# Kernel optimization log

Hardware: AMD Instinct MI355X
Metric: run time of the kernel (lower is better)

## Reference

```python
import jax, jax.numpy as jnp
import numpy as np

B, L, D, H = 2, 4096, 128, 4


def setup_inputs() -> dict:
    key = jax.random.key(0)
    k_x, k_q, k_k, k_v, k_o = jax.random.split(key, 5)
    std = 0.02
    x = jax.random.normal(k_x, (B, L, D), dtype=jnp.float32)
    # torch nn.Linear(d_model, H*d_model).weight has shape [H*D, D]
    Wq = std * jax.random.normal(k_q, (H * D, D), dtype=jnp.float32)
    Wk = std * jax.random.normal(k_k, (H * D, D), dtype=jnp.float32)
    Wv = std * jax.random.normal(k_v, (H * D, D), dtype=jnp.float32)
    # W_O: Linear(H*d_model, d_model).weight -> [D, H*D]
    Wo = std * jax.random.normal(k_o, (D, H * D), dtype=jnp.float32)
    return {"x": x, "Wq": Wq, "Wk": Wk, "Wv": Wv, "Wo": Wo}


def reference(x, Wq, Wk, Wv, Wo):
    # project: weight rows indexed by (h, e); out = x @ W^T
    Wq3 = Wq.reshape(H, D, D)
    Wk3 = Wk.reshape(H, D, D)
    Wv3 = Wv.reshape(H, D, D)
    q = jnp.einsum('bld,hed->bhle', x, Wq3)  # [B,H,L,D]
    k = jnp.einsum('bld,hed->bhle', x, Wk3)
    v = jnp.einsum('bld,hed->bhle', x, Wv3)
    logits = jnp.einsum('bhle,bhme->bhlm', q, k)  # [B,H,L,L]
    causal_mask = jnp.triu(jnp.ones((L, L), dtype=bool), 1)
    neg = jnp.finfo(logits.dtype).min
    logits = jnp.where(causal_mask, neg, logits)
    attn = jax.nn.softmax(logits, axis=-1)
    ctx = jnp.einsum('bhlm,bhme->bhle', attn, v)  # [B,H,L,D]
    ctx = ctx.transpose(0, 2, 1, 3).reshape(B, L, H * D)
    y = ctx @ Wo.T  # [B,L,D]
    return y
```

## Files before the change

### kernel.cpp

```cpp
#include <hip/hip_runtime.h>
#include <hip/hip_bf16.h>

#define BB 2
#define LL 4096
#define DD 128
#define HH 4

typedef unsigned short u16;
typedef unsigned int u32;
typedef __attribute__((ext_vector_type(8))) short short8;
typedef __attribute__((ext_vector_type(4))) float floatx4;

union PFrag { short8 s; u32 u[4]; };

__device__ __forceinline__ u16 f2bf(float f) {
    union { float f; u32 u; } v; v.f = f;
    return (u16)((v.u + 0x7fffu + ((v.u >> 16) & 1u)) >> 16);
}

__device__ __forceinline__ float bf2f(u16 u) {
    union { u32 u; float f; } v; v.u = (u32)u << 16;
    return v.f;
}

__device__ __forceinline__ u32 pk2bf(float a, float b) {
    union { __hip_bfloat162 h; u32 u; } v;
    v.h = __float22bfloat162_rn(float2{a, b});
    return v.u;
}

__device__ __forceinline__ void gld16(const u16* g, u16* l) {
    __builtin_amdgcn_global_load_lds((const __attribute__((address_space(1))) void*)g,
                                     (__attribute__((address_space(3))) void*)l, 16, 0, 0);
}

__device__ __forceinline__ int pfx2(int t) {
    int a = t >> 2, b = t & 3;
    return 2 * a * (a - 1) + a * b;
}

__global__ __launch_bounds__(256) void cvt_all(const float* __restrict__ x,
                                               const float* __restrict__ wq,
                                               const float* __restrict__ wk,
                                               const float* __restrict__ wv,
                                               const float* __restrict__ wo,
                                               u16* xb, u16* wqb, u16* wkb,
                                               u16* wvb, u16* wob,
                                               float* l_acc) {
    int z = blockIdx.y;
    if (z == 5) {
        int i = (blockIdx.x * 256 + threadIdx.x) * 4;
        if (i < 8 * LL) *(float4*)(l_acc + i) = (float4){0.f, 0.f, 0.f, 0.f};
        return;
    }
    const float* src; u16* dst; int n;
    if      (z == 0) { src = x;  dst = xb;  n = BB * LL * DD; }
    else if (z == 1) { src = wq; dst = wqb; n = HH * DD * DD; }
    else if (z == 2) { src = wk; dst = wkb; n = HH * DD * DD; }
    else if (z == 3) { src = wv; dst = wvb; n = HH * DD * DD; }
    else             { src = wo; dst = wob; n = DD * HH * DD; }
    int i = (blockIdx.x * 256 + threadIdx.x) * 4;
    if (i >= n) return;
    float4 v = *(const float4*)(src + i);
    ushort4 o;
    o.x = f2bf(v.x); o.y = f2bf(v.y); o.z = f2bf(v.z); o.w = f2bf(v.w);
    *(ushort4*)(dst + i) = o;
}

__global__ __launch_bounds__(256) void proj_qkv(const u16* __restrict__ xb,
                                                const u16* __restrict__ wqb,
                                                const u16* __restrict__ wkb,
                                                const u16* __restrict__ wvb,
                                                u16* __restrict__ Qb,
                                                u16* __restrict__ Kb,
                                                u16* __restrict__ Vt) {
    __shared__ __align__(16) u16 At[128 * 128];
    __shared__ __align__(16) u16 Wt[128 * 128];
    int lane = threadIdx.x & 63;
    int w    = threadIdx.x >> 6;
    int c = lane & 15, g = lane >> 4;
    int mt = blockIdx.x;
    int nt = blockIdx.y;
    int z = nt >> 2, h = nt & 3;
    const u16* Wg = ((z == 0) ? wqb : (z == 1) ? wkb : wvb) + h * 128 * DD;
    const u16* Ag = xb + (size_t)mt * 128 * DD;

#pragma unroll
    for (int i = 0; i < 8; i++) {
        int row = i * 16 + w * 4 + (lane >> 4);
        int cc  = (lane & 15) ^ (row & 15);
        gld16(Ag + row * DD + cc * 8, &At[(i * 16 + w * 4) * 128]);
    }
#pragma unroll
    for (int i = 0; i < 8; i++) {
        int row = i * 16 + w * 4 + (lane >> 4);
        int cc  = (lane & 15) ^ (row & 15);
        gld16(Wg + row * DD + cc * 8, &Wt[(i * 16 + w * 4) * 128]);
    }
    __syncthreads();

    const u16* Abuf = (z < 2) ? At : Wt;
    const u16* Bbuf = (z < 2) ? Wt : At;

    floatx4 acc[2][8];
#pragma unroll
    for (int m2 = 0; m2 < 2; m2++)
#pragma unroll
        for (int n2 = 0; n2 < 8; n2++) acc[m2][n2] = (floatx4){0.f, 0.f, 0.f, 0.f};

#pragma unroll
    for (int kk = 0; kk < 4; kk++) {
        short8 a0, a1, bf[8];
        {
            int r0 = w * 32 + c;
            int r1 = r0 + 16;
            a0 = *(const short8*)(&Abuf[r0 * 128 + (((g + 4 * kk) ^ (r0 & 15)) * 8)]);
            a1 = *(const short8*)(&Abuf[r1 * 128 + (((g + 4 * kk) ^ (r1 & 15)) * 8)]);
        }
#pragma unroll
        for (int n2 = 0; n2 < 8; n2++) {
            int rn = n2 * 16 + c;
            bf[n2] = *(const short8*)(&Bbuf[rn * 128 + (((g + 4 * kk) ^ (rn & 15)) * 8)]);
        }
#pragma unroll
        for (int n2 = 0; n2 < 8; n2++) {
            acc[0][n2] = __builtin_amdgcn_mfma_f32_16x16x32_bf16(a0, bf[n2], acc[0][n2], 0, 0, 0);
            acc[1][n2] = __builtin_amdgcn_mfma_f32_16x16x32_bf16(a1, bf[n2], acc[1][n2], 0, 0, 0);
        }
    }

    if (z < 2) {
        u16* out = (z == 0) ? Qb : Kb;
#pragma unroll
        for (int m2 = 0; m2 < 2; m2++)
#pragma unroll
            for (int r = 0; r < 4; r++) {
                int lg = mt * 128 + w * 32 + m2 * 16 + g * 4 + r;
                int b_ = lg >> 12, l = lg & 4095;
                u16* op = out + ((size_t)(b_ * HH + h) * LL + l) * DD + c;
#pragma unroll
                for (int n2 = 0; n2 < 8; n2++) op[n2 * 16] = f2bf(acc[m2][n2][r]);
            }
    } else {
        int b_ = mt >> 5;
        int lbase = (mt & 31) * 128;
#pragma unroll
        for (int m2 = 0; m2 < 2; m2++)
#pragma unroll
            for (int r = 0; r < 4; r++) {
                int e = w * 32 + m2 * 16 + g * 4 + r;
                u16* op = Vt + ((size_t)(b_ * HH + h) * DD + e) * LL + lbase + c;
#pragma unroll
                for (int n2 = 0; n2 < 8; n2++) op[n2 * 16] = f2bf(acc[m2][n2][r]);
            }
    }
}

__global__ __launch_bounds__(256, 3) void flash_attn(const u16* __restrict__ Q,
                                                     const u16* __restrict__ K,
                                                     const u16* __restrict__ Vt,
                                                     u16* __restrict__ basep,
                                                     u16* __restrict__ slots,
                                                     float* __restrict__ l_acc) {
    __shared__ __align__(16) u16 Kls[2][32 * 128];
    __shared__ __align__(16) u16 Vls[2][512 * 8];

    int lane = threadIdx.x & 63;
    int w    = threadIdx.x >> 6;
    int c = lane & 15, g = lane >> 4;

    int bid  = blockIdx.x;
    int head = bid & 7;
    int i    = bid >> 3;
    int t, ch;
    if (i < 120) {
        int rem = i; ch = 0;
        while (rem >= 29 - 4 * ch) { rem -= 29 - 4 * ch; ch++; }
        t = 31 - rem;
    } else {
        int j = i - 120;
        if (j < 8)       { t = 30 - 4 * j;        ch = (t - 2) >> 2; }
        else if (j < 16) { t = 29 - 4 * (j - 8);  ch = (t - 1) >> 2; }
        else             { t = 28 - 4 * (j - 16); ch = t >> 2; }
    }

    int kstart = ch << 9;
    int kend   = min((t + 1) << 7, kstart + 512);
    int nsteps = (kend - kstart) >> 5;

    int qb = t * 128 + w * 32;
    int my_steps = min(nsteps, ((qb + 31 - kstart) >> 5) + 1);

    short8 bq0[4], bq1[4];
    {
        const u16* qp0 = Q + ((size_t)head * LL + qb + c) * DD + g * 8;
        const u16* qp1 = qp0 + 16 * DD;
#pragma unroll
        for (int kk = 0; kk < 4; kk++) {
            bq0[kk] = *(const short8*)(qp0 + kk * 32);
            bq1[kk] = *(const short8*)(qp1 + kk * 32);
        }
    }

    floatx4 o0[8], o1[8];
#pragma unroll
    for (int tt = 0; tt < 8; tt++) {
        o0[tt] = (floatx4){0.f, 0.f, 0.f, 0.f};
        o1[tt] = (floatx4){0.f, 0.f, 0.f, 0.f};
    }
    float lsum0 = 0.f, lsum1 = 0.f;

    int s0 = c + (((g << 1) & 3) << 4);
    int s1 = c + ((((g << 1) | 1) & 3) << 4);
    bool hi = (g >= 2);

    const u16* Kg0 = K  + ((size_t)head * LL + kstart) * DD;
    const u16* Vg0 = Vt + (size_t)head * DD * LL + kstart;

    int q0 = w * 64 + lane;
    int r0 = q0 >> 4, cc0 = (q0 & 15) ^ (r0 & 15);
    int r1 = r0 + 16,  cc1 = (q0 & 15) ^ (r1 & 15);
    int ve  = q0 & 127;
    int vka = (q0 >> 7) * 8;

#define STAGE(s) {                                                          \
        int buf_ = (s) & 1; int kb_ = (s) << 5;                             \
        const u16* Kg = Kg0 + (size_t)kb_ * DD;                             \
        const u16* Vg = Vg0 + kb_;                                          \
        gld16(Kg + r0 * DD + cc0 * 8, &Kls[buf_][w * 512]);                 \
        gld16(Kg + r1 * DD + cc1 * 8, &Kls[buf_][2048 + w * 512]);          \
        gld16(Vg + (size_t)ve * LL + vka,      &Vls[buf_][w * 512]);        \
        gld16(Vg + (size_t)ve * LL + vka + 16, &Vls[buf_][2048 + w * 512]); \
    }

    STAGE(0);

    for (int j = 0; j < nsteps; ++j) {
        __syncthreads();
        if (j + 1 < nsteps) STAGE(j + 1);
        if (j < my_steps) {
            int kb = kstart + (j << 5);
            const u16* Kb_ = &Kls[j & 1][0];
            const u16* Vb_ = &Vls[j & 1][0];

            floatx4 st00 = {0,0,0,0}, st01 = {0,0,0,0};
            floatx4 st10 = {0,0,0,0}, st11 = {0,0,0,0};
            {
                short8 ka[4];
#pragma unroll
                for (int kk = 0; kk < 4; kk++)
                    ka[kk] = *(const short8*)(Kb_ + c * 128 + (((g + 4 * kk) ^ c)) * 8);
#pragma unroll
                for (int kk = 0; kk < 4; kk++) {
                    st00 = __builtin_amdgcn_mfma_f32_16x16x32_bf16(ka[kk], bq0[kk], st00, 0, 0, 0);
                    st10 = __builtin_amdgcn_mfma_f32_16x16x32_bf16(ka[kk], bq1[kk], st10, 0, 0, 0);
                }
#pragma unroll
                for (int kk = 0; kk < 4; kk++)
                    ka[kk] = *(const short8*)(Kb_ + (16 + c) * 128 + (((g + 4 * kk) ^ c)) * 8);
#pragma unroll
                for (int kk = 0; kk < 4; kk++) {
                    st01 = __builtin_amdgcn_mfma_f32_16x16x32_bf16(ka[kk], bq0[kk], st01, 0, 0, 0);
                    st11 = __builtin_amdgcn_mfma_f32_16x16x32_bf16(ka[kk], bq1[kk], st11, 0, 0, 0);
                }
            }

            PFrag au0, au1;
#pragma unroll
            for (int qh = 0; qh < 2; qh++) {
                floatx4 sa = qh ? st10 : st00;
                floatx4 sb = qh ? st11 : st01;
                int qbh = qb + qh * 16;
                float p[8];
                if (kb + 31 > qbh) {
                    int q_c = qbh + c;
#pragma unroll
                    for (int r = 0; r < 4; r++) {
                        int k0 = kb + g * 4 + r;
                        p[r]     = (k0      <= q_c) ? sa[r] : -INFINITY;
                        p[4 + r] = (k0 + 16 <= q_c) ? sb[r] : -INFINITY;
                    }
                } else {
#pragma unroll
                    for (int r = 0; r < 4; r++) { p[r] = sa[r]; p[4 + r] = sb[r]; }
                }
                float ls = 0.f;
#pragma unroll
                for (int i2 = 0; i2 < 8; i2++) { p[i2] = __expf(p[i2]); ls += p[i2]; }
                if (qh) lsum1 += ls; else lsum0 += ls;

                u32 pk00 = pk2bf(p[0], p[1]);
                u32 pk01 = pk2bf(p[2], p[3]);
                u32 pk10 = pk2bf(p[4], p[5]);
                u32 pk11 = pk2bf(p[6], p[7]);
                u32 x00 = (u32)__shfl((int)pk00, s0), x10 = (u32)__shfl((int)pk10, s0);
                u32 x01 = (u32)__shfl((int)pk01, s0), x11 = (u32)__shfl((int)pk11, s0);
                u32 y00 = (u32)__shfl((int)pk00, s1), y10 = (u32)__shfl((int)pk10, s1);
                u32 y01 = (u32)__shfl((int)pk01, s1), y11 = (u32)__shfl((int)pk11, s1);
                PFrag* au = qh ? &au1 : &au0;
                au->u[0] = hi ? x10 : x00;
                au->u[1] = hi ? x11 : x01;
                au->u[2] = hi ? y10 : y00;
                au->u[3] = hi ? y11 : y01;
            }

#pragma unroll
            for (int tt = 0; tt < 8; tt++) {
                short8 vb = *(const short8*)(Vb_ + g * 1024 + tt * 128 + c * 8);
                o0[tt] = __builtin_amdgcn_mfma_f32_16x16x32_bf16(au0.s, vb, o0[tt], 0, 0, 0);
                o1[tt] = __builtin_amdgcn_mfma_f32_16x16x32_bf16(au1.s, vb, o1[tt], 0, 0, 0);
            }
        }
    }
#undef STAGE

    lsum0 += __shfl_xor(lsum0, 16); lsum0 += __shfl_xor(lsum0, 32);
    lsum1 += __shfl_xor(lsum1, 16); lsum1 += __shfl_xor(lsum1, 32);
    if (g == 0) {
        atomicAdd(&l_acc[head * LL + qb + c],      lsum0);
        atomicAdd(&l_acc[head * LL + qb + 16 + c], lsum1);
    }

    bool diag = (kstart + 512 >= ((t + 1) << 7));
    u16* dst0 = diag ? basep + ((size_t)head * LL + t * 128) * 128
                     : slots + ((size_t)(head * 112 + pfx2(t) + ch)) * 16384;
    dst0 += (size_t)(w * 32) * 128;
#pragma unroll
    for (int r = 0; r < 4; r++) {
        u16* d0 = dst0 + (g * 4 + r) * 128 + c;
        u16* d1 = d0 + 16 * 128;
#pragma unroll
        for (int tt = 0; tt < 8; tt++) {
            d0[tt * 16] = f2bf(o0[tt][r]);
            d1[tt * 16] = f2bf(o1[tt][r]);
        }
    }
}

__global__ __launch_bounds__(256) void norm_cast(const u16* __restrict__ basep,
                                                 const u16* __restrict__ slots,
                                                 const float* __restrict__ l_acc,
                                                 u16* __restrict__ ctx) {
    int i = blockIdx.x * 256 + threadIdx.x;
    int e4 = i * 4;
    int col = e4 & 511;
    int bl  = e4 >> 9;
    int b_ = bl >> 12, l = bl & 4095;
    int h = col >> 7, d = col & 127;
    int head = b_ * HH + h;
    int t = l >> 7;
    int nx = t >> 2;

    ushort4 bv = *(const ushort4*)(basep + ((size_t)head * LL + l) * 128 + d);
    float v0 = bf2f(bv.x), v1 = bf2f(bv.y), v2 = bf2f(bv.z), v3 = bf2f(bv.w);
    if (nx > 0) {
        int sb = head * 112 + pfx2(t);
        for (int x = 0; x < nx; x++) {
            ushort4 sv = *(const ushort4*)(slots + (size_t)(sb + x) * 16384 + (l & 127) * 128 + d);
            v0 += bf2f(sv.x); v1 += bf2f(sv.y); v2 += bf2f(sv.z); v3 += bf2f(sv.w);
        }
    }
    float inv = 1.f / l_acc[head * LL + l];
    ushort4 o;
    o.x = f2bf(v0 * inv); o.y = f2bf(v1 * inv);
    o.z = f2bf(v2 * inv); o.w = f2bf(v3 * inv);
    *(ushort4*)(ctx + e4) = o;
}

__global__ __launch_bounds__(256) void proj_out(const u16* __restrict__ ctx,
                                                const u16* __restrict__ wo,
                                                float* __restrict__ y) {
    __shared__ __align__(16) u16 At[2][128 * 64];
    __shared__ __align__(16) u16 Wt[2][128 * 64];
    int lane = threadIdx.x & 63;
    int w    = threadIdx.x >> 6;
    int c = lane & 15, g = lane >> 4;
    int mt = blockIdx.x;
    const u16* Ag = ctx + (size_t)mt * 128 * 512;

#define PSTAGE(kc) {                                                        \
        int buf_ = (kc) & 1; int ks_ = (kc) * 64;                           \
        _Pragma("unroll")                                                   \
        for (int i = 0; i < 4; i++) {                                       \
            int row = i * 32 + w * 8 + (lane >> 3);                         \
            int cc  = (lane & 7) ^ (row & 7);                               \
            gld16(Ag + (size_t)row * 512 + ks_ + cc * 8,                    \
                  &At[buf_][(i * 32 + w * 8) * 64]);                        \
            gld16(wo + (size_t)row * 512 + ks_ + cc * 8,                    \
                  &Wt[buf_][(i * 32 + w * 8) * 64]);                        \
        }                                                                   \
    }

    floatx4 acc[2][8];
#pragma unroll
    for (int m2 = 0; m2 < 2; m2++)
#pragma unroll
        for (int n2 = 0; n2 < 8; n2++) acc[m2][n2] = (floatx4){0.f, 0.f, 0.f, 0.f};

    PSTAGE(0);
    for (int kc = 0; kc < 8; kc++) {
        __syncthreads();
        if (kc + 1 < 8) PSTAGE(kc + 1);
        int buf = kc & 1;
#pragma unroll
        for (int kk = 0; kk < 2; kk++) {
            int G = g + 4 * kk;
            short8 a0, a1, bf[8];
            {
                int ra = w * 32 + c;
                int rb = ra + 16;
                a0 = *(const short8*)(&At[buf][ra * 64 + ((G ^ (ra & 7)) * 8)]);
                a1 = *(const short8*)(&At[buf][rb * 64 + ((G ^ (rb & 7)) * 8)]);
            }
#pragma unroll
            for (int n2 = 0; n2 < 8; n2++) {
                int rn = n2 * 16 + c;
                bf[n2] = *(const short8*)(&Wt[buf][rn * 64 + ((G ^ (rn & 7)) * 8)]);
            }
#pragma unroll
            for (int n2 = 0; n2 < 8; n2++) {
                acc[0][n2] = __builtin_amdgcn_mfma_f32_16x16x32_bf16(a0, bf[n2], acc[0][n2], 0, 0, 0);
                acc[1][n2] = __builtin_amdgcn_mfma_f32_16x16x32_bf16(a1, bf[n2], acc[1][n2], 0, 0, 0);
            }
        }
    }
#undef PSTAGE

#pragma unroll
    for (int m2 = 0; m2 < 2; m2++)
#pragma unroll
        for (int r = 0; r < 4; r++) {
            int m = mt * 128 + w * 32 + m2 * 16 + g * 4 + r;
            float* yp = y + (size_t)m * 128 + c;
#pragma unroll
            for (int n2 = 0; n2 < 8; n2++) yp[n2 * 16] = acc[m2][n2][r];
        }
}

extern "C" void kernel_launch(void* const* d_in, const int* in_sizes, int n_in,
                              void* d_out, int out_size, void* d_ws, size_t ws_size,
                              hipStream_t stream) {
    const float* x  = (const float*)d_in[0];
    const float* Wq = (const float*)d_in[1];
    const float* Wk = (const float*)d_in[2];
    const float* Wv = (const float*)d_in[3];
    const float* Wo = (const float*)d_in[4];
    float* y = (float*)d_out;

    u16* ws  = (u16*)d_ws;
    u16* xb  = ws;
    u16* wqb = xb  + BB * LL * DD;
    u16* wkb = wqb + HH * DD * DD;
    u16* wvb = wkb + HH * DD * DD;
    u16* wob = wvb + HH * DD * DD;
    u16* Qb  = wob + DD * HH * DD;
    u16* Kb  = Qb  + BB * HH * LL * DD;
    u16* Vt  = Kb  + BB * HH * LL * DD;
    u16* ctx = Vt  + BB * HH * LL * DD;
    u16* basep = ctx + (size_t)BB * LL * HH * DD;
    u16* slots = basep + (size_t)8 * LL * 128;
    float* l_acc = (float*)(slots + (size_t)896 * 16384);

    cvt_all<<<dim3(1024, 6), 256, 0, stream>>>(x, Wq, Wk, Wv, Wo,
                                               xb, wqb, wkb, wvb, wob, l_acc);
    proj_qkv<<<dim3(64, 12), 256, 0, stream>>>(xb, wqb, wkb, wvb, Qb, Kb, Vt);
    flash_attn<<<dim3(1152), 256, 0, stream>>>(Qb, Kb, Vt, basep, slots, l_acc);
    norm_cast<<<dim3(4096), 256, 0, stream>>>(basep, slots, l_acc, ctx);
    proj_out<<<dim3(64), 256, 0, stream>>>(ctx, wob, y);
}
```

Before: 151.7 us.

## Fuse split-K reduction and normalization into output projection kernel

```diff
diff --git a/kernel.cpp b/kernel.cpp
--- a/kernel.cpp
+++ b/kernel.cpp
@@ -12,6 +12,7 @@
 typedef __attribute__((ext_vector_type(4))) float floatx4;
 
 union PFrag { short8 s; u32 u[4]; };
+union BF8 { short8 s; u16 h[8]; };
 
 __device__ __forceinline__ u16 f2bf(float f) {
     union { float f; u32 u; } v; v.f = f;
@@ -337,104 +338,104 @@
     }
 }
 
-__global__ __launch_bounds__(256) void norm_cast(const u16* __restrict__ basep,
-                                                 const u16* __restrict__ slots,
-                                                 const float* __restrict__ l_acc,
-                                                 u16* __restrict__ ctx) {
-    int i = blockIdx.x * 256 + threadIdx.x;
-    int e4 = i * 4;
-    int col = e4 & 511;
-    int bl  = e4 >> 9;
-    int b_ = bl >> 12, l = bl & 4095;
-    int h = col >> 7, d = col & 127;
-    int head = b_ * HH + h;
-    int t = l >> 7;
-    int nx = t >> 2;
-
-    ushort4 bv = *(const ushort4*)(basep + ((size_t)head * LL + l) * 128 + d);
-    float v0 = bf2f(bv.x), v1 = bf2f(bv.y), v2 = bf2f(bv.z), v3 = bf2f(bv.w);
-    if (nx > 0) {
-        int sb = head * 112 + pfx2(t);
-        for (int x = 0; x < nx; x++) {
-            ushort4 sv = *(const ushort4*)(slots + (size_t)(sb + x) * 16384 + (l & 127) * 128 + d);
-            v0 += bf2f(sv.x); v1 += bf2f(sv.y); v2 += bf2f(sv.z); v3 += bf2f(sv.w);
-        }
-    }
-    float inv = 1.f / l_acc[head * LL + l];
-    ushort4 o;
-    o.x = f2bf(v0 * inv); o.y = f2bf(v1 * inv);
-    o.z = f2bf(v2 * inv); o.w = f2bf(v3 * inv);
-    *(ushort4*)(ctx + e4) = o;
-}
-
-__global__ __launch_bounds__(256) void proj_out(const u16* __restrict__ ctx,
+__global__ __launch_bounds__(256) void proj_out(const u16* __restrict__ basep,
+                                                const u16* __restrict__ slots,
+                                                const float* __restrict__ l_acc,
                                                 const u16* __restrict__ wo,
                                                 float* __restrict__ y) {
-    __shared__ __align__(16) u16 At[2][128 * 64];
-    __shared__ __align__(16) u16 Wt[2][128 * 64];
-    int lane = threadIdx.x & 63;
-    int w    = threadIdx.x >> 6;
+    __shared__ __align__(16) u16 Als[2][64 * 64];
+    __shared__ __align__(16) u16 Wls[2][128 * 64];
+    int tid  = threadIdx.x;
+    int lane = tid & 63;
+    int w    = tid >> 6;
     int c = lane & 15, g = lane >> 4;
-    int mt = blockIdx.x;
-    const u16* Ag = ctx + (size_t)mt * 128 * 512;
-
-#define PSTAGE(kc) {                                                        \
-        int buf_ = (kc) & 1; int ks_ = (kc) * 64;                           \
-        _Pragma("unroll")                                                   \
-        for (int i = 0; i < 4; i++) {                                       \
-            int row = i * 32 + w * 8 + (lane >> 3);                         \
-            int cc  = (lane & 7) ^ (row & 7);                               \
-            gld16(Ag + (size_t)row * 512 + ks_ + cc * 8,                    \
-                  &At[buf_][(i * 32 + w * 8) * 64]);                        \
-            gld16(wo + (size_t)row * 512 + ks_ + cc * 8,                    \
-                  &Wt[buf_][(i * 32 + w * 8) * 64]);                        \
-        }                                                                   \
-    }
-
-    floatx4 acc[2][8];
-#pragma unroll
-    for (int m2 = 0; m2 < 2; m2++)
-#pragma unroll
-        for (int n2 = 0; n2 < 8; n2++) acc[m2][n2] = (floatx4){0.f, 0.f, 0.f, 0.f};
-
-    PSTAGE(0);
+    int mt2 = blockIdx.x;
+    int rowbase = mt2 * 64;
+    int b_ = rowbase >> 12;
+    int lbase = rowbase & 4095;
+    int t = lbase >> 7;
+    int nx = t >> 2;
+
+    int arow = tid >> 2;
+    int l    = lbase + arow;
+    int lrow = l & 127;
+    float inv4[4];
+#pragma unroll
+    for (int h = 0; h < 4; h++) inv4[h] = 1.f / l_acc[(b_ * HH + h) * LL + l];
+
+#define ASTAGE(kc) {                                                          \
+        int buf_ = (kc) & 1;                                                  \
+        int h_ = (kc) >> 1;                                                   \
+        int head_ = b_ * HH + h_;                                             \
+        float inv_ = inv4[h_];                                                \
+        int sbh = head_ * 112 + pfx2(t);                                      \
+        _Pragma("unroll")                                                     \
+        for (int s = 0; s < 2; s++) {                                         \
+            int u = (tid & 3) * 2 + s;                                        \
+            int dglob = ((kc) & 1) * 64 + u * 8;                              \
+            BF8 bv; bv.s = *(const short8*)(basep +                           \
+                ((size_t)head_ * LL + l) * 128 + dglob);                      \
+            float v[8];                                                       \
+            _Pragma("unroll")                                                 \
+            for (int e = 0; e < 8; e++) v[e] = bf2f(bv.h[e]);                 \
+            for (int x = 0; x < nx; x++) {                                    \
+                BF8 sv; sv.s = *(const short8*)(slots +                       \
+                    (size_t)(sbh + x) * 16384 + lrow * 128 + dglob);          \
+                _Pragma("unroll")                                             \
+                for (int e = 0; e < 8; e++) v[e] += bf2f(sv.h[e]);            \
+            }                                                                 \
+            BF8 ov;                                                           \
+            _Pragma("unroll")                                                 \
+            for (int e = 0; e < 8; e++) ov.h[e] = f2bf(v[e] * inv_);          \
+            *(short8*)(&Als[buf_][arow * 64 + ((u ^ (arow & 7)) * 8)]) = ov.s;\
+        }                                                                     \
+    }
+
+#define WSTAGE(kc) {                                                          \
+        int buf_ = (kc) & 1; int ks_ = (kc) * 64;                             \
+        _Pragma("unroll")                                                     \
+        for (int i = 0; i < 4; i++) {                                         \
+            int row = i * 32 + (tid >> 3);                                    \
+            int cc  = (tid & 7) ^ (row & 7);                                  \
+            gld16(wo + (size_t)row * 512 + ks_ + cc * 8,                      \
+                  &Wls[buf_][i * 2048 + w * 512]);                            \
+        }                                                                     \
+    }
+
+    floatx4 acc[8];
+#pragma unroll
+    for (int n2 = 0; n2 < 8; n2++) acc[n2] = (floatx4){0.f, 0.f, 0.f, 0.f};
+
+    ASTAGE(0); WSTAGE(0);
+#pragma unroll
     for (int kc = 0; kc < 8; kc++) {
         __syncthreads();
-        if (kc + 1 < 8) PSTAGE(kc + 1);
+        if (kc + 1 < 8) { ASTAGE(kc + 1); WSTAGE(kc + 1); }
         int buf = kc & 1;
 #pragma unroll
         for (int kk = 0; kk < 2; kk++) {
             int G = g + 4 * kk;
-            short8 a0, a1, bf[8];
-            {
-                int ra = w * 32 + c;
-                int rb = ra + 16;
-                a0 = *(const short8*)(&At[buf][ra * 64 + ((G ^ (ra & 7)) * 8)]);
-                a1 = *(const short8*)(&At[buf][rb * 64 + ((G ^ (rb & 7)) * 8)]);
-            }
-#pragma unroll
-            for (int n2 = 0; n2 < 8; n2++) {
-                int rn = n2 * 16 + c;
-                bf[n2] = *(const short8*)(&Wt[buf][rn * 64 + ((G ^ (rn & 7)) * 8)]);
-            }
-#pragma unroll
-            for (int n2 = 0; n2 < 8; n2++) {
-                acc[0][n2] = __builtin_amdgcn_mfma_f32_16x16x32_bf16(a0, bf[n2], acc[0][n2], 0, 0, 0);
-                acc[1][n2] = __builtin_amdgcn_mfma_f32_16x16x32_bf16(a1, bf[n2], acc[1][n2], 0, 0, 0);
-            }
-        }
-    }
-#undef PSTAGE
-
-#pragma unroll
-    for (int m2 = 0; m2 < 2; m2++)
-#pragma unroll
-        for (int r = 0; r < 4; r++) {
-            int m = mt * 128 + w * 32 + m2 * 16 + g * 4 + r;
-            float* yp = y + (size_t)m * 128 + c;
-#pragma unroll
-            for (int n2 = 0; n2 < 8; n2++) yp[n2 * 16] = acc[m2][n2][r];
-        }
+            int sw = (G ^ (c & 7)) * 8;
+            short8 a0 = *(const short8*)(&Als[buf][(w * 16 + c) * 64 + sw]);
+            short8 bf[8];
+#pragma unroll
+            for (int n2 = 0; n2 < 8; n2++)
+                bf[n2] = *(const short8*)(&Wls[buf][(n2 * 16 + c) * 64 + sw]);
+#pragma unroll
+            for (int n2 = 0; n2 < 8; n2++)
+                acc[n2] = __builtin_amdgcn_mfma_f32_16x16x32_bf16(a0, bf[n2], acc[n2], 0, 0, 0);
+        }
+    }
+#undef ASTAGE
+#undef WSTAGE
+
+#pragma unroll
+    for (int r = 0; r < 4; r++) {
+        int m = rowbase + w * 16 + g * 4 + r;
+        float* yp = y + (size_t)m * 128 + c;
+#pragma unroll
+        for (int n2 = 0; n2 < 8; n2++) yp[n2 * 16] = acc[n2][r];
+    }
 }
 
 extern "C" void kernel_launch(void* const* d_in, const int* in_sizes, int n_in,
@@ -456,8 +457,7 @@
     u16* Qb  = wob + DD * HH * DD;
     u16* Kb  = Qb  + BB * HH * LL * DD;
     u16* Vt  = Kb  + BB * HH * LL * DD;
-    u16* ctx = Vt  + BB * HH * LL * DD;
-    u16* basep = ctx + (size_t)BB * LL * HH * DD;
+    u16* basep = Vt + (size_t)BB * HH * LL * DD;
     u16* slots = basep + (size_t)8 * LL * 128;
     float* l_acc = (float*)(slots + (size_t)896 * 16384);
 
@@ -465,6 +465,5 @@
                                                xb, wqb, wkb, wvb, wob, l_acc);
     proj_qkv<<<dim3(64, 12), 256, 0, stream>>>(xb, wqb, wkb, wvb, Qb, Kb, Vt);
     flash_attn<<<dim3(1152), 256, 0, stream>>>(Qb, Kb, Vt, basep, slots, l_acc);
-    norm_cast<<<dim3(4096), 256, 0, stream>>>(basep, slots, l_acc, ctx);
-    proj_out<<<dim3(64), 256, 0, stream>>>(ctx, wob, y);
-}
+    proj_out<<<dim3(128), 256, 0, stream>>>(basep, slots, l_acc, wob, y);
+}
```

New measurement: 168.6 us. +11.1%, slower.

## Fuse fp32-to-bf16 conversion into projection kernels and drop cvt_all

Applied to the files above, without the earlier changes.

```diff
diff --git a/kernel.cpp b/kernel.cpp
--- a/kernel.cpp
+++ b/kernel.cpp
@@ -39,120 +39,102 @@
     return 2 * a * (a - 1) + a * b;
 }
 
-__global__ __launch_bounds__(256) void cvt_all(const float* __restrict__ x,
-                                               const float* __restrict__ wq,
-                                               const float* __restrict__ wk,
-                                               const float* __restrict__ wv,
-                                               const float* __restrict__ wo,
-                                               u16* xb, u16* wqb, u16* wkb,
-                                               u16* wvb, u16* wob,
-                                               float* l_acc) {
-    int z = blockIdx.y;
-    if (z == 5) {
-        int i = (blockIdx.x * 256 + threadIdx.x) * 4;
-        if (i < 8 * LL) *(float4*)(l_acc + i) = (float4){0.f, 0.f, 0.f, 0.f};
-        return;
-    }
-    const float* src; u16* dst; int n;
-    if      (z == 0) { src = x;  dst = xb;  n = BB * LL * DD; }
-    else if (z == 1) { src = wq; dst = wqb; n = HH * DD * DD; }
-    else if (z == 2) { src = wk; dst = wkb; n = HH * DD * DD; }
-    else if (z == 3) { src = wv; dst = wvb; n = HH * DD * DD; }
-    else             { src = wo; dst = wob; n = DD * HH * DD; }
-    int i = (blockIdx.x * 256 + threadIdx.x) * 4;
-    if (i >= n) return;
-    float4 v = *(const float4*)(src + i);
-    ushort4 o;
-    o.x = f2bf(v.x); o.y = f2bf(v.y); o.z = f2bf(v.z); o.w = f2bf(v.w);
-    *(ushort4*)(dst + i) = o;
-}
-
-__global__ __launch_bounds__(256) void proj_qkv(const u16* __restrict__ xb,
-                                                const u16* __restrict__ wqb,
-                                                const u16* __restrict__ wkb,
-                                                const u16* __restrict__ wvb,
+__device__ __forceinline__ void stage_tile_f32(const float* __restrict__ g,
+                                               u16* lds, int tid) {
+#pragma unroll
+    for (int it = 0; it < 8; it++) {
+        int unit = it * 256 + tid;
+        int row = unit >> 4, uu = unit & 15;
+        const float4* gp = (const float4*)(g + (size_t)row * 128 + uu * 8);
+        float4 f0 = gp[0], f1 = gp[1];
+        PFrag pv;
+        pv.u[0] = pk2bf(f0.x, f0.y); pv.u[1] = pk2bf(f0.z, f0.w);
+        pv.u[2] = pk2bf(f1.x, f1.y); pv.u[3] = pk2bf(f1.z, f1.w);
+        *(short8*)(&lds[row * 128 + ((uu ^ (row & 15)) * 8)]) = pv.s;
+    }
+}
+
+__global__ __launch_bounds__(256) void proj_qkv(const float* __restrict__ x,
+                                                const float* __restrict__ wq,
+                                                const float* __restrict__ wk,
+                                                const float* __restrict__ wv,
                                                 u16* __restrict__ Qb,
                                                 u16* __restrict__ Kb,
                                                 u16* __restrict__ Vt) {
     __shared__ __align__(16) u16 At[128 * 128];
-    __shared__ __align__(16) u16 Wt[128 * 128];
-    int lane = threadIdx.x & 63;
-    int w    = threadIdx.x >> 6;
+    __shared__ __align__(16) u16 Wt[2][128 * 128];
+    int tid  = threadIdx.x;
+    int lane = tid & 63;
+    int w    = tid >> 6;
     int c = lane & 15, g = lane >> 4;
     int mt = blockIdx.x;
-    int nt = blockIdx.y;
-    int z = nt >> 2, h = nt & 3;
-    const u16* Wg = ((z == 0) ? wqb : (z == 1) ? wkb : wvb) + h * 128 * DD;
-    const u16* Ag = xb + (size_t)mt * 128 * DD;
-
-#pragma unroll
-    for (int i = 0; i < 8; i++) {
-        int row = i * 16 + w * 4 + (lane >> 4);
-        int cc  = (lane & 15) ^ (row & 15);
-        gld16(Ag + row * DD + cc * 8, &At[(i * 16 + w * 4) * 128]);
-    }
-#pragma unroll
-    for (int i = 0; i < 8; i++) {
-        int row = i * 16 + w * 4 + (lane >> 4);
-        int cc  = (lane & 15) ^ (row & 15);
-        gld16(Wg + row * DD + cc * 8, &Wt[(i * 16 + w * 4) * 128]);
-    }
+    int h  = blockIdx.y;
+
+    stage_tile_f32(x  + (size_t)mt * 128 * 128, At,    tid);
+    stage_tile_f32(wq + (size_t)h  * 128 * 128, Wt[0], tid);
     __syncthreads();
 
-    const u16* Abuf = (z < 2) ? At : Wt;
-    const u16* Bbuf = (z < 2) ? Wt : At;
-
-    floatx4 acc[2][8];
-#pragma unroll
-    for (int m2 = 0; m2 < 2; m2++)
-#pragma unroll
-        for (int n2 = 0; n2 < 8; n2++) acc[m2][n2] = (floatx4){0.f, 0.f, 0.f, 0.f};
-
-#pragma unroll
-    for (int kk = 0; kk < 4; kk++) {
-        short8 a0, a1, bf[8];
-        {
-            int r0 = w * 32 + c;
-            int r1 = r0 + 16;
-            a0 = *(const short8*)(&Abuf[r0 * 128 + (((g + 4 * kk) ^ (r0 & 15)) * 8)]);
-            a1 = *(const short8*)(&Abuf[r1 * 128 + (((g + 4 * kk) ^ (r1 & 15)) * 8)]);
-        }
-#pragma unroll
-        for (int n2 = 0; n2 < 8; n2++) {
-            int rn = n2 * 16 + c;
-            bf[n2] = *(const short8*)(&Bbuf[rn * 128 + (((g + 4 * kk) ^ (rn & 15)) * 8)]);
-        }
-#pragma unroll
-        for (int n2 = 0; n2 < 8; n2++) {
-            acc[0][n2] = __builtin_amdgcn_mfma_f32_16x16x32_bf16(a0, bf[n2], acc[0][n2], 0, 0, 0);
-            acc[1][n2] = __builtin_amdgcn_mfma_f32_16x16x32_bf16(a1, bf[n2], acc[1][n2], 0, 0, 0);
-        }
-    }
-
-    if (z < 2) {
-        u16* out = (z == 0) ? Qb : Kb;
+#pragma unroll
+    for (int z = 0; z < 3; z++) {
+        if (z == 0) stage_tile_f32(wk + (size_t)h * 128 * 128, Wt[1], tid);
+        if (z == 1) stage_tile_f32(wv + (size_t)h * 128 * 128, Wt[0], tid);
+        const u16* Wcur = Wt[z & 1];
+        const u16* Abuf = (z < 2) ? At : Wcur;
+        const u16* Bbuf = (z < 2) ? Wcur : At;
+
+        floatx4 acc[2][8];
 #pragma unroll
         for (int m2 = 0; m2 < 2; m2++)
 #pragma unroll
-            for (int r = 0; r < 4; r++) {
-                int lg = mt * 128 + w * 32 + m2 * 16 + g * 4 + r;
-                int b_ = lg >> 12, l = lg & 4095;
-                u16* op = out + ((size_t)(b_ * HH + h) * LL + l) * DD + c;
-#pragma unroll
-                for (int n2 = 0; n2 < 8; n2++) op[n2 * 16] = f2bf(acc[m2][n2][r]);
-            }
-    } else {
-        int b_ = mt >> 5;
-        int lbase = (mt & 31) * 128;
-#pragma unroll
-        for (int m2 = 0; m2 < 2; m2++)
-#pragma unroll
-            for (int r = 0; r < 4; r++) {
-                int e = w * 32 + m2 * 16 + g * 4 + r;
-                u16* op = Vt + ((size_t)(b_ * HH + h) * DD + e) * LL + lbase + c;
-#pragma unroll
-                for (int n2 = 0; n2 < 8; n2++) op[n2 * 16] = f2bf(acc[m2][n2][r]);
-            }
+            for (int n2 = 0; n2 < 8; n2++) acc[m2][n2] = (floatx4){0.f, 0.f, 0.f, 0.f};
+
+#pragma unroll
+        for (int kk = 0; kk < 4; kk++) {
+            short8 a0, a1, bf[8];
+            {
+                int r0 = w * 32 + c;
+                int r1 = r0 + 16;
+                a0 = *(const short8*)(&Abuf[r0 * 128 + (((g + 4 * kk) ^ (r0 & 15)) * 8)]);
+                a1 = *(const short8*)(&Abuf[r1 * 128 + (((g + 4 * kk) ^ (r1 & 15)) * 8)]);
+            }
+#pragma unroll
+            for (int n2 = 0; n2 < 8; n2++) {
+                int rn = n2 * 16 + c;
+                bf[n2] = *(const short8*)(&Bbuf[rn * 128 + (((g + 4 * kk) ^ (rn & 15)) * 8)]);
+            }
+#pragma unroll
+            for (int n2 = 0; n2 < 8; n2++) {
+                acc[0][n2] = __builtin_amdgcn_mfma_f32_16x16x32_bf16(a0, bf[n2], acc[0][n2], 0, 0, 0);
+                acc[1][n2] = __builtin_amdgcn_mfma_f32_16x16x32_bf16(a1, bf[n2], acc[1][n2], 0, 0, 0);
+            }
+        }
+
+        if (z < 2) {
+            u16* out = (z == 0) ? Qb : Kb;
+#pragma unroll
+            for (int m2 = 0; m2 < 2; m2++)
+#pragma unroll
+                for (int r = 0; r < 4; r++) {
+                    int lg = mt * 128 + w * 32 + m2 * 16 + g * 4 + r;
+                    int b_ = lg >> 12, l = lg & 4095;
+                    u16* op = out + ((size_t)(b_ * HH + h) * LL + l) * DD + c;
+#pragma unroll
+                    for (int n2 = 0; n2 < 8; n2++) op[n2 * 16] = f2bf(acc[m2][n2][r]);
+                }
+        } else {
+            int b_ = mt >> 5;
+            int lbase = (mt & 31) * 128;
+#pragma unroll
+            for (int m2 = 0; m2 < 2; m2++)
+#pragma unroll
+                for (int r = 0; r < 4; r++) {
+                    int e = w * 32 + m2 * 16 + g * 4 + r;
+                    u16* op = Vt + ((size_t)(b_ * HH + h) * DD + e) * LL + lbase + c;
+#pragma unroll
+                    for (int n2 = 0; n2 < 8; n2++) op[n2 * 16] = f2bf(acc[m2][n2][r]);
+                }
+        }
+        __syncthreads();
     }
 }
 
@@ -368,12 +350,13 @@
 }
 
 __global__ __launch_bounds__(256) void proj_out(const u16* __restrict__ ctx,
-                                                const u16* __restrict__ wo,
+                                                const float* __restrict__ wo,
                                                 float* __restrict__ y) {
     __shared__ __align__(16) u16 At[2][128 * 64];
     __shared__ __align__(16) u16 Wt[2][128 * 64];
-    int lane = threadIdx.x & 63;
-    int w    = threadIdx.x >> 6;
+    int tid  = threadIdx.x;
+    int lane = tid & 63;
+    int w    = tid >> 6;
     int c = lane & 15, g = lane >> 4;
     int mt = blockIdx.x;
     const u16* Ag = ctx + (size_t)mt * 128 * 512;
@@ -386,8 +369,18 @@
             int cc  = (lane & 7) ^ (row & 7);                               \
             gld16(Ag + (size_t)row * 512 + ks_ + cc * 8,                    \
                   &At[buf_][(i * 32 + w * 8) * 64]);                        \
-            gld16(wo + (size_t)row * 512 + ks_ + cc * 8,                    \
-                  &Wt[buf_][(i * 32 + w * 8) * 64]);                        \
+        }                                                                   \
+        _Pragma("unroll")                                                   \
+        for (int it = 0; it < 4; it++) {                                    \
+            int unit = it * 256 + tid;                                      \
+            int row = unit >> 3, uu = unit & 7;                             \
+            const float4* gp = (const float4*)(wo + (size_t)row * 512 +     \
+                                               ks_ + uu * 8);               \
+            float4 f0 = gp[0], f1 = gp[1];                                  \
+            PFrag pv;                                                       \
+            pv.u[0] = pk2bf(f0.x, f0.y); pv.u[1] = pk2bf(f0.z, f0.w);       \
+            pv.u[2] = pk2bf(f1.x, f1.y); pv.u[3] = pk2bf(f1.z, f1.w);       \
+            *(short8*)(&Wt[buf_][row * 64 + ((uu ^ (row & 7)) * 8)]) = pv.s;\
         }                                                                   \
     }
 
@@ -448,23 +441,18 @@
     float* y = (float*)d_out;
 
     u16* ws  = (u16*)d_ws;
-    u16* xb  = ws;
-    u16* wqb = xb  + BB * LL * DD;
-    u16* wkb = wqb + HH * DD * DD;
-    u16* wvb = wkb + HH * DD * DD;
-    u16* wob = wvb + HH * DD * DD;
-    u16* Qb  = wob + DD * HH * DD;
-    u16* Kb  = Qb  + BB * HH * LL * DD;
-    u16* Vt  = Kb  + BB * HH * LL * DD;
-    u16* ctx = Vt  + BB * HH * LL * DD;
+    u16* Qb  = ws;
+    u16* Kb  = Qb + (size_t)BB * HH * LL * DD;
+    u16* Vt  = Kb + (size_t)BB * HH * LL * DD;
+    u16* ctx = Vt + (size_t)BB * HH * LL * DD;
     u16* basep = ctx + (size_t)BB * LL * HH * DD;
     u16* slots = basep + (size_t)8 * LL * 128;
     float* l_acc = (float*)(slots + (size_t)896 * 16384);
 
-    cvt_all<<<dim3(1024, 6), 256, 0, stream>>>(x, Wq, Wk, Wv, Wo,
-                                               xb, wqb, wkb, wvb, wob, l_acc);
-    proj_qkv<<<dim3(64, 12), 256, 0, stream>>>(xb, wqb, wkb, wvb, Qb, Kb, Vt);
+    (void)hipMemsetAsync(l_acc, 0, (size_t)8 * LL * 4, stream);
+
+    proj_qkv<<<dim3(64, 4), 256, 0, stream>>>(x, Wq, Wk, Wv, Qb, Kb, Vt);
     flash_attn<<<dim3(1152), 256, 0, stream>>>(Qb, Kb, Vt, basep, slots, l_acc);
     norm_cast<<<dim3(4096), 256, 0, stream>>>(basep, slots, l_acc, ctx);
-    proj_out<<<dim3(64), 256, 0, stream>>>(ctx, wob, y);
-}
+    proj_out<<<dim3(64), 256, 0, stream>>>(ctx, Wo, y);
+}
```

Measured after the change: 153.6 us. About the same (+1.2%).
